# Optimization experiments

Measured on AMD Instinct MI355X. Metric: run time of the kernel, lower is better.

The kernel has to match this reference:

```python
import jax, jax.numpy as jnp
import numpy as np

K_UPPER = 196608  # number of smallest-|grad| positions to mask per sample


def setup_inputs() -> dict:
    key = jax.random.key(0)
    k1, k2 = jax.random.split(key)
    x = jax.random.normal(k1, (64, 3, 512, 512), dtype=jnp.float32)
    grad = jax.random.normal(k2, (64, 3, 512, 512), dtype=jnp.float32)
    return {"x": x, "grad": grad}


def _mask_low_gradient(x, grad):
    # x, grad: [B, C, H, W]
    B, C, H, W = x.shape
    hw = H * W
    flat_g = grad.reshape(B, -1)                                  # [B, C*H*W]
    # _sort: k smallest absolute gradients -> top_k of negated abs (unsorted ok)
    _neg_vals, idx = jax.lax.top_k(-jnp.abs(flat_g), K_UPPER)     # idx: [B, K]
    # channel containing each selected flat index (matches the torch range test)
    ch = idx // hw                                                # [B, K]
    xc = x.reshape(B, C, hw)
    # Faithful to source: torch slice [start:channel_indexes] EXCLUDES the last
    # element of each channel when computing min/max.
    mn = jnp.min(xc[:, :, : hw - 1], axis=-1)                     # [B, C]
    mx = jnp.max(xc[:, :, : hw - 1], axis=-1)                     # [B, C]
    lo = jnp.take_along_axis(mn, ch, axis=1)                      # [B, K]
    hi = jnp.take_along_axis(mx, ch, axis=1)                      # [B, K]
    # uniform fill in [lo, hi) per masked element
    u = jax.random.uniform(jax.random.key(42), idx.shape, dtype=x.dtype)
    fill = lo + u * (hi - lo)                                     # [B, K]
    flat_x = x.reshape(B, -1)
    out = flat_x.at[jnp.arange(B)[:, None], idx].set(fill)
    return out.reshape(x.shape)


def reference(x, grad):
    return _mask_low_gradient(x, grad)
```

## Files before the change

### kernel.cpp

```cpp
#include <hip/hip_runtime.h>
#include <stdint.h>

#define TPB 256
#define TPS 1024

constexpr int BN   = 64;
constexpr int CCH  = 3;
constexpr int HWS  = 262144;
constexpr int LOG_HW = 18;
constexpr int NPS  = 786432;
constexpr int KSEL = 196608;
constexpr int KCAP = 200704;
constexpr int NB_T = 32;
constexpr int CH_T = NPS / NB_T;
constexpr int NB_C = 64;
constexpr int CH_C = NPS / NB_C;
constexpr int NB_S = 8;
constexpr int CH_S = KCAP / NB_S;
constexpr int TILE = 4096;
constexpr int NBINS = 2048;
constexpr int SUB  = 8;

constexpr int WS_MN   = 0;
constexpr int WS_MX   = 192;
constexpr int WS_V1   = 384;
constexpr int WS_B1   = 448;
constexpr int WS_GS   = 512;
constexpr int WS_KP   = 576;
constexpr int WS_CNT  = 640;
constexpr int WS_COFF = WS_CNT + BN * NB_C;
constexpr int WS_MNP  = WS_COFF + BN * NB_C;
constexpr int WS_MXP  = WS_MNP + BN * CCH * SUB;
constexpr int WS_THA  = WS_MXP + BN * CCH * SUB;
constexpr int WS_THB  = WS_THA + BN * NBINS;
constexpr int WS_H0   = WS_THB + BN * NBINS;
constexpr int WS_H1   = WS_H0 + BN * 256 * NB_S;
constexpr int WS_H2   = WS_H1 + BN * 256 * NB_S;
constexpr int WS_H3   = WS_H2 + BN * 256 * NB_S;
constexpr size_t WS_FIX_END = (size_t)WS_H3 + (size_t)BN * 256 * NB_S;
constexpr size_t RECW = (size_t)BN * KCAP * 2;
constexpr size_t WS_NEEDED_BYTES = (WS_FIX_END + 2 * RECW) * 4;

__device__ __forceinline__ unsigned rotl32(unsigned x, int r) { return (x << r) | (x >> (32 - r)); }

__device__ __forceinline__ void tf4(unsigned& x0, unsigned& x1, int a, int b, int c, int d) {
  x0 += x1; x1 = rotl32(x1, a); x1 ^= x0;
  x0 += x1; x1 = rotl32(x1, b); x1 ^= x0;
  x0 += x1; x1 = rotl32(x1, c); x1 ^= x0;
  x0 += x1; x1 = rotl32(x1, d); x1 ^= x0;
}

__device__ __forceinline__ void threefry2x32(unsigned k0, unsigned k1, unsigned c0, unsigned c1,
                                             unsigned& o0, unsigned& o1) {
  const unsigned ks2 = k0 ^ k1 ^ 0x1BD11BDAu;
  unsigned x0 = c0 + k0, x1 = c1 + k1;
  tf4(x0, x1, 13, 15, 26, 6);  x0 += k1;  x1 += ks2 + 1u;
  tf4(x0, x1, 17, 29, 16, 24); x0 += ks2; x1 += k0 + 2u;
  tf4(x0, x1, 13, 15, 26, 6);  x0 += k0;  x1 += k1 + 3u;
  tf4(x0, x1, 17, 29, 16, 24); x0 += k1;  x1 += ks2 + 4u;
  tf4(x0, x1, 13, 15, 26, 6);  x0 += ks2; x1 += k0 + 5u;
  o0 = x0; o1 = x1;
}

__global__ __launch_bounds__(TPB) void k_zero(unsigned* __restrict__ p, int n) {
  int i = blockIdx.x * TPB + threadIdx.x;
  if (i < n) p[i] = 0u;
}

__global__ __launch_bounds__(TPB) void k_mnmx(const float4* __restrict__ x,
                                              unsigned* __restrict__ ws) {
  __shared__ float smn[TPB], smx[TPB];
  const int g = blockIdx.x;
  const int bc = g / SUB, sub = g - bc * SUB;
  const int Q4 = HWS / 4 / SUB;
  const size_t base4 = (size_t)bc * (HWS / 4) + (size_t)sub * Q4;
  const bool last = (sub == SUB - 1);
  const int tid = threadIdx.x;
  float lo = 3.4e38f, hi = -3.4e38f;
  for (int i = tid; i < Q4; i += TPB) {
    float4 v = x[base4 + i];
    if (last && i == Q4 - 1) {
      lo = fminf(lo, fminf(fminf(v.x, v.y), v.z));
      hi = fmaxf(hi, fmaxf(fmaxf(v.x, v.y), v.z));
    } else {
      lo = fminf(lo, fminf(fminf(v.x, v.y), fminf(v.z, v.w)));
      hi = fmaxf(hi, fmaxf(fmaxf(v.x, v.y), fmaxf(v.z, v.w)));
    }
  }
  smn[tid] = lo; smx[tid] = hi; __syncthreads();
  for (int s = TPB / 2; s > 0; s >>= 1) {
    if (tid < s) { smn[tid] = fminf(smn[tid], smn[tid + s]); smx[tid] = fmaxf(smx[tid], smx[tid + s]); }
    __syncthreads();
  }
  if (tid == 0) {
    ((float*)(ws + WS_MNP))[g] = smn[0];
    ((float*)(ws + WS_MXP))[g] = smx[0];
  }
}

__global__ __launch_bounds__(TPB) void k_mnfin(unsigned* __restrict__ ws) {
  const int t = threadIdx.x;
  if (t < BN * CCH) {
    const float* mnp = (const float*)(ws + WS_MNP);
    const float* mxp = (const float*)(ws + WS_MXP);
    float lo = 3.4e38f, hi = -3.4e38f;
    for (int s = 0; s < SUB; ++s) {
      lo = fminf(lo, mnp[t * SUB + s]);
      hi = fmaxf(hi, mxp[t * SUB + s]);
    }
    ((float*)(ws + WS_MN))[t] = lo;
    ((float*)(ws + WS_MX))[t] = hi;
  }
}

__global__ __launch_bounds__(TPB) void k_thrA(const unsigned* __restrict__ gb, unsigned* __restrict__ hist) {
  __shared__ unsigned h[NBINS];
  const int b = blockIdx.y, blk = blockIdx.x, tid = threadIdx.x;
  for (int v = tid; v < NBINS; v += TPB) h[v] = 0u;
  __syncthreads();
  const uint4* g4 = (const uint4*)(gb + (size_t)b * NPS + (size_t)blk * CH_T);
  for (int i = tid; i < CH_T / 4; i += TPB) {
    uint4 v = g4[i];
    atomicAdd(&h[(v.x & 0x7FFFFFFFu) >> 21], 1u);
    atomicAdd(&h[(v.y & 0x7FFFFFFFu) >> 21], 1u);
    atomicAdd(&h[(v.z & 0x7FFFFFFFu) >> 21], 1u);
    atomicAdd(&h[(v.w & 0x7FFFFFFFu) >> 21], 1u);
  }
  __syncthreads();
  unsigned* gh = hist + (size_t)b * NBINS;
  for (int v = tid; v < NBINS; v += TPB) if (h[v]) atomicAdd(&gh[v], h[v]);
}

__global__ __launch_bounds__(TPB) void k_thrB(const unsigned* __restrict__ gb,
                                              unsigned* __restrict__ hist,
                                              const unsigned* __restrict__ ws) {
  __shared__ unsigned h[NBINS];
  const int b = blockIdx.y, blk = blockIdx.x, tid = threadIdx.x;
  for (int v = tid; v < NBINS; v += TPB) h[v] = 0u;
  __syncthreads();
  const unsigned sel = ws[WS_V1 + b];
  const uint4* g4 = (const uint4*)(gb + (size_t)b * NPS + (size_t)blk * CH_T);
  for (int i = tid; i < CH_T / 4; i += TPB) {
    uint4 v = g4[i];
    unsigned a0 = v.x & 0x7FFFFFFFu, a1 = v.y & 0x7FFFFFFFu;
    unsigned a2 = v.z & 0x7FFFFFFFu, a3 = v.w & 0x7FFFFFFFu;
    if ((a0 >> 21) == sel) atomicAdd(&h[(a0 >> 10) & 2047u], 1u);
    if ((a1 >> 21) == sel) atomicAdd(&h[(a1 >> 10) & 2047u], 1u);
    if ((a2 >> 21) == sel) atomicAdd(&h[(a2 >> 10) & 2047u], 1u);
    if ((a3 >> 21) == sel) atomicAdd(&h[(a3 >> 10) & 2047u], 1u);
  }
  __syncthreads();
  unsigned* gh = hist + (size_t)b * NBINS;
  for (int v = tid; v < NBINS; v += TPB) if (h[v]) atomicAdd(&gh[v], h[v]);
}

__global__ __launch_bounds__(TPB) void k_find(const unsigned* __restrict__ hist,
                                              unsigned* __restrict__ ws, int mode) {
  __shared__ unsigned part[TPB];
  const int b = blockIdx.x, tid = threadIdx.x;
  const unsigned* h = hist + (size_t)b * NBINS;
  const int per = NBINS / TPB;
  const unsigned Kt = (mode == 0) ? (unsigned)KSEL : (unsigned)KSEL - ws[WS_B1 + b];
  unsigned vals[8];
  unsigned s = 0;
  for (int j = 0; j < per; ++j) { vals[j] = h[tid * per + j]; s += vals[j]; }
  part[tid] = s; __syncthreads();
  for (int off = 1; off < TPB; off <<= 1) {
    unsigned t = (tid >= off) ? part[tid - off] : 0u;
    __syncthreads(); part[tid] += t; __syncthreads();
  }
  unsigned run = part[tid] - s;
  for (int j = 0; j < per; ++j) {
    const unsigned lo = run, c = vals[j];
    run += c;
    if (lo < Kt && Kt <= run) {
      const unsigned v = (unsigned)(tid * per + j);
      if (mode == 0) {
        ws[WS_V1 + b] = v; ws[WS_B1 + b] = lo;
      } else {
        const unsigned T22 = (ws[WS_V1 + b] << 11) | v;
        ws[WS_GS + b] = (T22 << 10) | 1023u;
        unsigned kp = ws[WS_B1 + b] + lo + c;
        if (kp > (unsigned)KCAP) kp = (unsigned)KCAP;
        ws[WS_KP + b] = kp;
      }
    }
  }
}

__global__ __launch_bounds__(TPB) void k_ccount(const unsigned* __restrict__ gb, unsigned* __restrict__ ws) {
  __shared__ unsigned r[TPB];
  const int b = blockIdx.y, blk = blockIdx.x, tid = threadIdx.x;
  const unsigned G = ws[WS_GS + b];
  const uint4* g4 = (const uint4*)(gb + (size_t)b * NPS + (size_t)blk * CH_C);
  unsigned c = 0;
  for (int i = tid; i < CH_C / 4; i += TPB) {
    uint4 v = g4[i];
    c += (unsigned)((v.x & 0x7FFFFFFFu) <= G) + (unsigned)((v.y & 0x7FFFFFFFu) <= G)
       + (unsigned)((v.z & 0x7FFFFFFFu) <= G) + (unsigned)((v.w & 0x7FFFFFFFu) <= G);
  }
  r[tid] = c; __syncthreads();
  for (int s = TPB / 2; s > 0; s >>= 1) { if (tid < s) r[tid] += r[tid + s]; __syncthreads(); }
  if (tid == 0) ws[WS_CNT + b * NB_C + blk] = r[0];
}

__global__ void k_cscan(unsigned* __restrict__ ws) {
  const int b = blockIdx.x;
  if (threadIdx.x == 0) {
    unsigned run = 0;
    for (int j = 0; j < NB_C; ++j) {
      unsigned t = ws[WS_CNT + b * NB_C + j];
      ws[WS_COFF + b * NB_C + j] = run;
      run += t;
    }
  }
}

__global__ __launch_bounds__(TPB) void k_cscatter(const unsigned* __restrict__ gb,
                                                  const unsigned* __restrict__ ws,
                                                  unsigned* __restrict__ keyArr,
                                                  unsigned* __restrict__ H0) {
  __shared__ unsigned h2[256 * NB_S];
  __shared__ unsigned waveTot[4];
  __shared__ unsigned runBase;
  const int b = blockIdx.y, blk = blockIdx.x, tid = threadIdx.x;
  const int lane = tid & 63, wv = tid >> 6;
  const unsigned G = ws[WS_GS + b];
  for (int e = tid; e < 256 * NB_S; e += TPB) h2[e] = 0u;
  if (tid == 0) runBase = ws[WS_COFF + b * NB_C + blk];
  __syncthreads();
  const uint4* g4 = (const uint4*)(gb + (size_t)b * NPS + (size_t)blk * CH_C);
  unsigned* ka = keyArr + (size_t)b * KCAP;
  for (int t = 0; t < CH_C / 1024; ++t) {
    const uint4 v = g4[t * 256 + tid];
    unsigned k[4] = { v.x & 0x7FFFFFFFu, v.y & 0x7FFFFFFFu, v.z & 0x7FFFFFFFu, v.w & 0x7FFFFFFFu };
    bool s[4];
    unsigned cnt = 0;
#pragma unroll
    for (int c = 0; c < 4; ++c) { s[c] = (k[c] <= G); cnt += (unsigned)s[c]; }
    unsigned incl = cnt;
    for (int off = 1; off < 64; off <<= 1) {
      unsigned u = __shfl_up(incl, off, 64);
      if (lane >= off) incl += u;
    }
    if (lane == 63) waveTot[wv] = incl;
    __syncthreads();
    const unsigned wt0 = waveTot[0], wt1 = waveTot[1], wt2 = waveTot[2], wt3 = waveTot[3];
    unsigned wpre = 0;
    if (wv > 0) wpre += wt0;
    if (wv > 1) wpre += wt1;
    if (wv > 2) wpre += wt2;
    unsigned pos = runBase + wpre + (incl - cnt);
#pragma unroll
    for (int c = 0; c < 4; ++c) {
      if (s[c]) {
        if (pos < (unsigned)KCAP) {
          ka[pos] = k[c];
          atomicAdd(&h2[(k[c] & 255u) * NB_S + pos / (unsigned)CH_S], 1u);
        }
        ++pos;
      }
    }
    __syncthreads();
    if (tid == 0) runBase += wt0 + wt1 + wt2 + wt3;
  }
  __syncthreads();
  unsigned* Hb = H0 + (size_t)b * 256 * NB_S;
  for (int e = tid; e < 256 * NB_S; e += TPB) {
    unsigned c = h2[e];
    if (c) atomicAdd(&Hb[e], c);
  }
}

__global__ __launch_bounds__(TPB) void k_hscan(unsigned* __restrict__ H) {
  __shared__ unsigned wsum[4];
  const int b = blockIdx.x, tid = threadIdx.x;
  const int lane = tid & 63, wv = tid >> 6;
  unsigned* Hb = H + (size_t)b * 256 * NB_S;
  unsigned row[NB_S];
  unsigned run = 0;
#pragma unroll
  for (int k = 0; k < NB_S; ++k) {
    unsigned t = Hb[tid * NB_S + k];
    row[k] = run; run += t;
  }
  unsigned incl = run;
  for (int off = 1; off < 64; off <<= 1) {
    unsigned t = __shfl_up(incl, off, 64);
    if (lane >= off) incl += t;
  }
  if (lane == 63) wsum[wv] = incl;
  __syncthreads();
  unsigned wpre = 0;
  for (int w = 0; w < wv; ++w) wpre += wsum[w];
  const unsigned excl = incl - run + wpre;
#pragma unroll
  for (int k = 0; k < NB_S; ++k) Hb[tid * NB_S + k] = row[k] + excl;
}

template<int MODE>
__global__ __launch_bounds__(TPS) void k_sort8(const unsigned* __restrict__ keyIn,
                                               const uint2* __restrict__ inR,
                                               uint2* __restrict__ outR,
                                               unsigned* __restrict__ fillmap,
                                               const unsigned* __restrict__ Hcur,
                                               unsigned* __restrict__ Hnext,
                                               const unsigned* __restrict__ ws,
                                               int shift) {
  __shared__ unsigned wh[16][256];
  __shared__ unsigned gout[256];
  __shared__ unsigned gbase[256];
  __shared__ unsigned wsum[4];
  __shared__ uint2    stg[(MODE == 2) ? 1 : TILE];
  __shared__ unsigned h2[(MODE == 2) ? 1 : 256 * NB_S];
  const int b = blockIdx.y, blk = blockIdx.x, tid = threadIdx.x;
  const int lane = tid & 63, wv = tid >> 6;
  const unsigned long long ltm = (1ull << lane) - 1ull;
  const unsigned kp = min(ws[WS_KP + b], (unsigned)KCAP);
  const unsigned s0 = (unsigned)blk * CH_S;
  const unsigned s1 = min(s0 + (unsigned)CH_S, kp);
  const unsigned* ki = keyIn + (size_t)b * KCAP;
  const uint2* in = inR + (size_t)b * KCAP;
  uint2* out = outR + (size_t)b * KCAP;
  unsigned* fm = fillmap + (size_t)b * KCAP;

  for (int d = tid; d < 256; d += TPS) gbase[d] = Hcur[((size_t)b * 256 + d) * NB_S + blk];
  if (MODE != 2) for (int e = tid; e < 256 * NB_S; e += TPS) h2[e] = 0u;
  __syncthreads();

  for (unsigned t0 = s0; t0 < s1; t0 += (unsigned)TILE) {
    { uint4* w4 = (uint4*)&wh[0][0];
      w4[tid] = make_uint4(0u, 0u, 0u, 0u); }
    __syncthreads();

    unsigned key[4], cpp[4], wloc[4], dig[4];
    bool val[4];
    const unsigned wbase = t0 + (unsigned)wv * 256u;
#pragma unroll
    for (int c = 0; c < 4; ++c) {
      const unsigned i = wbase + (unsigned)c * 64u + (unsigned)lane;
      val[c] = (i < s1);
      if (MODE == 0) { cpp[c] = i; key[c] = val[c] ? ki[i] : 0u; }
      else { uint2 r = val[c] ? in[i] : make_uint2(0u, 0u); cpp[c] = r.x; key[c] = r.y; }
      dig[c] = (key[c] >> shift) & 255u;
      unsigned long long peers = __ballot(val[c]);
#pragma unroll
      for (int bit = 0; bit < 8; ++bit) {
        unsigned long long bb = __ballot(val[c] && ((dig[c] >> bit) & 1u));
        peers &= ((dig[c] >> bit) & 1u) ? bb : ~bb;
      }
      const unsigned before = (unsigned)__popcll(peers & ltm);
      int ldr = __ffsll((unsigned long long)peers) - 1;
      if (ldr < 0) ldr = 0;
      unsigned old = 0;
      if (val[c] && lane == ldr) old = atomicAdd(&wh[wv][dig[c]], (unsigned)__popcll(peers));
      old = __shfl(old, ldr, 64);
      wloc[c] = old + before;
    }
    __syncthreads();

    unsigned incl = 0, tot = 0;
    if (tid < 256) {
      const unsigned d = (unsigned)tid;
#pragma unroll
      for (int w = 0; w < 16; ++w) tot += wh[w][d];
      incl = tot;
      for (int off = 1; off < 64; off <<= 1) {
        unsigned t = __shfl_up(incl, off, 64);
        if (lane >= off) incl += t;
      }
      if (lane == 63) wsum[wv] = incl;
    }
    __syncthreads();
    if (tid < 256) {
      const unsigned d = (unsigned)tid;
      unsigned wpre = 0;
      for (int w = 0; w < wv; ++w) wpre += wsum[w];
      const unsigned tstart = incl - tot + wpre;
      const unsigned g = gbase[d];
      gout[d] = g - tstart;
      gbase[d] = g + tot;
      unsigned run = tstart;
#pragma unroll
      for (int w = 0; w < 16; ++w) { const unsigned t = wh[w][d]; wh[w][d] = run; run += t; }
    }
    __syncthreads();

    if (MODE != 2) {
#pragma unroll
      for (int c = 0; c < 4; ++c) {
        if (val[c]) {
          uint2 r; r.x = cpp[c]; r.y = key[c];
          stg[wh[wv][dig[c]] + wloc[c]] = r;
        }
      }
      __syncthreads();
      const unsigned nt = min((unsigned)TILE, s1 - t0);
      for (unsigned j = tid; j < nt; j += TPS) {
        const uint2 r = stg[j];
        const unsigned d = (r.y >> shift) & 255u;
        const unsigned pos = gout[d] + j;
        out[pos] = r;
        const unsigned nd = (r.y >> (shift + 8)) & 255u;
        atomicAdd(&h2[nd * NB_S + pos / (unsigned)CH_S], 1u);
      }
    } else {
#pragma unroll
      for (int c = 0; c < 4; ++c) {
        if (val[c]) {
          const unsigned rank = gout[dig[c]] + wh[wv][dig[c]] + wloc[c];
          fm[cpp[c]] = (rank < (unsigned)KSEL) ? rank : 0xFFFFFFFFu;
        }
      }
    }
    __syncthreads();
  }

  if (MODE != 2) {
    unsigned* Hb = Hnext + (size_t)b * 256 * NB_S;
    for (int e = tid; e < 256 * NB_S; e += TPS) {
      unsigned c = h2[e];
      if (c) atomicAdd(&Hb[e], c);
    }
  }
}

__global__ __launch_bounds__(TPB) void k_fill(const uint4* __restrict__ x4,
                                              const unsigned* __restrict__ gb,
                                              const unsigned* __restrict__ fillmap,
                                              const unsigned* __restrict__ ws,
                                              float4* __restrict__ out4) {
  __shared__ unsigned waveTot[4];
  __shared__ unsigned runBase;
  const int b = blockIdx.y, blk = blockIdx.x, tid = threadIdx.x;
  const int lane = tid & 63, wv = tid >> 6;
  const unsigned G = ws[WS_GS + b];
  const unsigned kp = min(ws[WS_KP + b], (unsigned)KCAP);
  if (tid == 0) runBase = ws[WS_COFF + b * NB_C + blk];
  __syncthreads();
  const size_t base4 = ((size_t)b * NPS + (size_t)blk * CH_C) / 4;
  const uint4* g4 = (const uint4*)(gb + (size_t)b * NPS + (size_t)blk * CH_C);
  const unsigned* fm = fillmap + (size_t)b * KCAP;
  const float* mnf = (const float*)(ws + WS_MN);
  const float* mxf = (const float*)(ws + WS_MX);
  const unsigned ebase = (unsigned)blk * (unsigned)CH_C;

  for (int t = 0; t < CH_C / 1024; ++t) {
    const uint4 gv = g4[t * 256 + tid];
    uint4 xv = ((const uint4*)x4)[base4 + t * 256 + tid];
    unsigned k[4] = { gv.x & 0x7FFFFFFFu, gv.y & 0x7FFFFFFFu, gv.z & 0x7FFFFFFFu, gv.w & 0x7FFFFFFFu };
    bool s[4];
    unsigned cnt = 0;
#pragma unroll
    for (int c = 0; c < 4; ++c) { s[c] = (k[c] <= G); cnt += (unsigned)s[c]; }
    unsigned incl = cnt;
    for (int off = 1; off < 64; off <<= 1) {
      unsigned u = __shfl_up(incl, off, 64);
      if (lane >= off) incl += u;
    }
    if (lane == 63) waveTot[wv] = incl;
    __syncthreads();
    const unsigned wt0 = waveTot[0], wt1 = waveTot[1], wt2 = waveTot[2], wt3 = waveTot[3];
    unsigned wpre = 0;
    if (wv > 0) wpre += wt0;
    if (wv > 1) wpre += wt1;
    if (wv > 2) wpre += wt2;
    unsigned pos = runBase + wpre + (incl - cnt);
    unsigned* xw = (unsigned*)&xv;
#pragma unroll
    for (int c = 0; c < 4; ++c) {
      if (s[c]) {
        if (pos < kp) {
          const unsigned r = fm[pos];
          if (r != 0xFFFFFFFFu) {
            const unsigned p = (unsigned)b * (unsigned)KSEL + r;
            unsigned o0, o1;
            threefry2x32(0u, 42u, 0u, p, o0, o1);
            const unsigned bits = o0 ^ o1;
            const float u = __uint_as_float((bits >> 9) | 0x3f800000u) - 1.0f;
            const unsigned e = ebase + (unsigned)t * 1024u + (unsigned)tid * 4u + (unsigned)c;
            const unsigned ch = e >> LOG_HW;
            const float lo = mnf[b * CCH + ch];
            const float hi = mxf[b * CCH + ch];
            xw[c] = __float_as_uint(lo + u * (hi - lo));
          }
        }
        ++pos;
      }
    }
    ((uint4*)out4)[base4 + t * 256 + tid] = xv;
    __syncthreads();
    if (tid == 0) runBase += wt0 + wt1 + wt2 + wt3;
  }
}

extern "C" void kernel_launch(void* const* d_in, const int* in_sizes, int n_in,
                              void* d_out, int out_size, void* d_ws, size_t ws_size,
                              hipStream_t stream) {
  const float* x = (const float*)d_in[0];
  const unsigned* gb = (const unsigned*)d_in[1];
  float* out = (float*)d_out;
  unsigned* ws = (unsigned*)d_ws;
  if (ws_size < WS_NEEDED_BYTES) return;

  unsigned* R1 = ws + WS_FIX_END;
  unsigned* R2 = ws + WS_FIX_END + RECW;
  unsigned* H0 = ws + WS_H0;
  unsigned* H1 = ws + WS_H1;
  unsigned* H2 = ws + WS_H2;
  unsigned* H3 = ws + WS_H3;

  dim3 blk(TPB);
  dim3 sblk(TPS);

  k_mnmx<<<dim3(BN * CCH * SUB), blk, 0, stream>>>((const float4*)x, ws);
  k_mnfin<<<dim3(1), blk, 0, stream>>>(ws);
  {
    const int nz = (int)(WS_FIX_END - WS_THA);
    k_zero<<<dim3((nz + TPB - 1) / TPB), blk, 0, stream>>>(ws + WS_THA, nz);
  }

  k_thrA<<<dim3(NB_T, BN), blk, 0, stream>>>(gb, ws + WS_THA);
  k_find<<<dim3(BN), blk, 0, stream>>>(ws + WS_THA, ws, 0);
  k_thrB<<<dim3(NB_T, BN), blk, 0, stream>>>(gb, ws + WS_THB, ws);
  k_find<<<dim3(BN), blk, 0, stream>>>(ws + WS_THB, ws, 1);

  k_ccount<<<dim3(NB_C, BN), blk, 0, stream>>>(gb, ws);
  k_cscan<<<dim3(BN), dim3(64), 0, stream>>>(ws);
  k_cscatter<<<dim3(NB_C, BN), blk, 0, stream>>>(gb, ws, R1, H0);

  k_hscan<<<dim3(BN), blk, 0, stream>>>(H0);
  k_sort8<0><<<dim3(NB_S, BN), sblk, 0, stream>>>(R1, (const uint2*)nullptr, (uint2*)R2, nullptr, H0, H1, ws, 0);
  k_hscan<<<dim3(BN), blk, 0, stream>>>(H1);
  k_sort8<1><<<dim3(NB_S, BN), sblk, 0, stream>>>(nullptr, (const uint2*)R2, (uint2*)R1, nullptr, H1, H2, ws, 8);
  k_hscan<<<dim3(BN), blk, 0, stream>>>(H2);
  k_sort8<1><<<dim3(NB_S, BN), sblk, 0, stream>>>(nullptr, (const uint2*)R1, (uint2*)R2, nullptr, H2, H3, ws, 16);
  k_hscan<<<dim3(BN), blk, 0, stream>>>(H3);
  k_sort8<2><<<dim3(NB_S, BN), sblk, 0, stream>>>(nullptr, (const uint2*)R2, (uint2*)nullptr, R1, H3, nullptr, ws, 24);

  k_fill<<<dim3(NB_C, BN), blk, 0, stream>>>((const uint4*)x, gb, R1, ws, (float4*)out);
}
```

Before: 798.2 us.

## Use per-wave compaction offsets and compute fill values in final sort pass

Compaction now gives each wave its own contiguous sub-chunk with a precomputed offset. This removes the two block-wide barriers per iteration in the scatter and fill kernels, and the single-thread scan becomes a parallel 256-entry scan. The threefry RNG and lo/hi fill computation move from k_fill into the last sort pass (MODE 2), which writes the final float value into the fillmap. Per-channel selected counts are accumulated so the sort pass can find each element's channel from its compacted position. This adds atomics in k_ccount and more arithmetic in the sort kernel, but k_fill becomes a plain memory-bound merge.

Result: faster. 779.5 us (-2.3%).

```diff
diff --git a/kernel.cpp b/kernel.cpp
--- a/kernel.cpp
+++ b/kernel.cpp
@@ -15,6 +15,7 @@
 constexpr int CH_T = NPS / NB_T;
 constexpr int NB_C = 64;
 constexpr int CH_C = NPS / NB_C;
+constexpr int WCH  = CH_C / 4;
 constexpr int NB_S = 8;
 constexpr int CH_S = KCAP / NB_S;
 constexpr int TILE = 4096;
@@ -27,11 +28,14 @@
 constexpr int WS_B1   = 448;
 constexpr int WS_GS   = 512;
 constexpr int WS_KP   = 576;
-constexpr int WS_CNT  = 640;
-constexpr int WS_COFF = WS_CNT + BN * NB_C;
-constexpr int WS_MNP  = WS_COFF + BN * NB_C;
+constexpr int WS_S0   = 640;
+constexpr int WS_S01  = 704;
+constexpr int WS_CNT  = 768;
+constexpr int WS_COFF = WS_CNT + BN * 256;
+constexpr int WS_MNP  = WS_COFF + BN * 256;
 constexpr int WS_MXP  = WS_MNP + BN * CCH * SUB;
-constexpr int WS_THA  = WS_MXP + BN * CCH * SUB;
+constexpr int WS_CHC  = WS_MXP + BN * CCH * SUB;
+constexpr int WS_THA  = WS_CHC + BN * 4;
 constexpr int WS_THB  = WS_THA + BN * NBINS;
 constexpr int WS_H0   = WS_THB + BN * NBINS;
 constexpr int WS_H1   = WS_H0 + BN * 256 * NB_S;
@@ -189,30 +193,56 @@
 }
 
 __global__ __launch_bounds__(TPB) void k_ccount(const unsigned* __restrict__ gb, unsigned* __restrict__ ws) {
-  __shared__ unsigned r[TPB];
+  __shared__ unsigned chs[3];
   const int b = blockIdx.y, blk = blockIdx.x, tid = threadIdx.x;
+  const int lane = tid & 63, wv = tid >> 6;
+  if (tid < 3) chs[tid] = 0u;
+  __syncthreads();
   const unsigned G = ws[WS_GS + b];
-  const uint4* g4 = (const uint4*)(gb + (size_t)b * NPS + (size_t)blk * CH_C);
-  unsigned c = 0;
-  for (int i = tid; i < CH_C / 4; i += TPB) {
-    uint4 v = g4[i];
-    c += (unsigned)((v.x & 0x7FFFFFFFu) <= G) + (unsigned)((v.y & 0x7FFFFFFFu) <= G)
-       + (unsigned)((v.z & 0x7FFFFFFFu) <= G) + (unsigned)((v.w & 0x7FFFFFFFu) <= G);
-  }
-  r[tid] = c; __syncthreads();
-  for (int s = TPB / 2; s > 0; s >>= 1) { if (tid < s) r[tid] += r[tid + s]; __syncthreads(); }
-  if (tid == 0) ws[WS_CNT + b * NB_C + blk] = r[0];
-}
-
-__global__ void k_cscan(unsigned* __restrict__ ws) {
-  const int b = blockIdx.x;
-  if (threadIdx.x == 0) {
-    unsigned run = 0;
-    for (int j = 0; j < NB_C; ++j) {
-      unsigned t = ws[WS_CNT + b * NB_C + j];
-      ws[WS_COFF + b * NB_C + j] = run;
-      run += t;
-    }
+  const uint4* g4 = (const uint4*)(gb + (size_t)b * NPS + (size_t)blk * CH_C) + wv * (WCH / 4);
+  const unsigned e0 = (unsigned)blk * CH_C + (unsigned)wv * WCH;
+  unsigned cnt = 0, cc0 = 0, cc1 = 0, cc2 = 0;
+  for (int it = 0; it < WCH / 256; ++it) {
+    const uint4 v = g4[it * 64 + lane];
+    const unsigned e = e0 + (unsigned)it * 256u + (unsigned)lane * 4u;
+    const unsigned k[4] = { v.x & 0x7FFFFFFFu, v.y & 0x7FFFFFFFu, v.z & 0x7FFFFFFFu, v.w & 0x7FFFFFFFu };
+#pragma unroll
+    for (int c = 0; c < 4; ++c) {
+      if (k[c] <= G) {
+        ++cnt;
+        const unsigned ch = (e + (unsigned)c) >> LOG_HW;
+        if (ch == 0) ++cc0; else if (ch == 1) ++cc1; else ++cc2;
+      }
+    }
+  }
+  for (int off = 32; off >= 1; off >>= 1) cnt += __shfl_down(cnt, off, 64);
+  if (lane == 0) ws[WS_CNT + b * 256 + blk * 4 + wv] = cnt;
+  if (cc0) atomicAdd(&chs[0], cc0);
+  if (cc1) atomicAdd(&chs[1], cc1);
+  if (cc2) atomicAdd(&chs[2], cc2);
+  __syncthreads();
+  if (tid < 3 && chs[tid]) atomicAdd(&ws[WS_CHC + b * 4 + tid], chs[tid]);
+}
+
+__global__ __launch_bounds__(TPB) void k_cscan(unsigned* __restrict__ ws) {
+  __shared__ unsigned wsum[4];
+  const int b = blockIdx.x, tid = threadIdx.x;
+  const int lane = tid & 63, wv = tid >> 6;
+  const unsigned cnt = ws[WS_CNT + b * 256 + tid];
+  unsigned incl = cnt;
+  for (int off = 1; off < 64; off <<= 1) {
+    unsigned t = __shfl_up(incl, off, 64);
+    if (lane >= off) incl += t;
+  }
+  if (lane == 63) wsum[wv] = incl;
+  __syncthreads();
+  unsigned wpre = 0;
+  for (int w = 0; w < wv; ++w) wpre += wsum[w];
+  ws[WS_COFF + b * 256 + tid] = incl - cnt + wpre;
+  if (tid == 0) {
+    const unsigned s0 = ws[WS_CHC + b * 4 + 0];
+    ws[WS_S0 + b] = s0;
+    ws[WS_S01 + b] = s0 + ws[WS_CHC + b * 4 + 1];
   }
 }
 
@@ -221,18 +251,16 @@
                                                   unsigned* __restrict__ keyArr,
                                                   unsigned* __restrict__ H0) {
   __shared__ unsigned h2[256 * NB_S];
-  __shared__ unsigned waveTot[4];
-  __shared__ unsigned runBase;
   const int b = blockIdx.y, blk = blockIdx.x, tid = threadIdx.x;
   const int lane = tid & 63, wv = tid >> 6;
+  for (int e = tid; e < 256 * NB_S; e += TPB) h2[e] = 0u;
+  __syncthreads();
   const unsigned G = ws[WS_GS + b];
-  for (int e = tid; e < 256 * NB_S; e += TPB) h2[e] = 0u;
-  if (tid == 0) runBase = ws[WS_COFF + b * NB_C + blk];
-  __syncthreads();
-  const uint4* g4 = (const uint4*)(gb + (size_t)b * NPS + (size_t)blk * CH_C);
+  unsigned base = ws[WS_COFF + b * 256 + blk * 4 + wv];
+  const uint4* g4 = (const uint4*)(gb + (size_t)b * NPS + (size_t)blk * CH_C) + wv * (WCH / 4);
   unsigned* ka = keyArr + (size_t)b * KCAP;
-  for (int t = 0; t < CH_C / 1024; ++t) {
-    const uint4 v = g4[t * 256 + tid];
+  for (int it = 0; it < WCH / 256; ++it) {
+    const uint4 v = g4[it * 64 + lane];
     unsigned k[4] = { v.x & 0x7FFFFFFFu, v.y & 0x7FFFFFFFu, v.z & 0x7FFFFFFFu, v.w & 0x7FFFFFFFu };
     bool s[4];
     unsigned cnt = 0;
@@ -243,14 +271,8 @@
       unsigned u = __shfl_up(incl, off, 64);
       if (lane >= off) incl += u;
     }
-    if (lane == 63) waveTot[wv] = incl;
-    __syncthreads();
-    const unsigned wt0 = waveTot[0], wt1 = waveTot[1], wt2 = waveTot[2], wt3 = waveTot[3];
-    unsigned wpre = 0;
-    if (wv > 0) wpre += wt0;
-    if (wv > 1) wpre += wt1;
-    if (wv > 2) wpre += wt2;
-    unsigned pos = runBase + wpre + (incl - cnt);
+    const unsigned wtot = __shfl(incl, 63, 64);
+    unsigned pos = base + incl - cnt;
 #pragma unroll
     for (int c = 0; c < 4; ++c) {
       if (s[c]) {
@@ -261,8 +283,7 @@
         ++pos;
       }
     }
-    __syncthreads();
-    if (tid == 0) runBase += wt0 + wt1 + wt2 + wt3;
+    base += wtot;
   }
   __syncthreads();
   unsigned* Hb = H0 + (size_t)b * 256 * NB_S;
@@ -324,6 +345,16 @@
   uint2* out = outR + (size_t)b * KCAP;
   unsigned* fm = fillmap + (size_t)b * KCAP;
 
+  unsigned S0 = 0, S01 = 0;
+  float l0 = 0, l1 = 0, l2 = 0, h0 = 0, h1 = 0, h2v = 0;
+  if (MODE == 2) {
+    S0 = ws[WS_S0 + b]; S01 = ws[WS_S01 + b];
+    const float* mnf = (const float*)(ws + WS_MN);
+    const float* mxf = (const float*)(ws + WS_MX);
+    l0 = mnf[b * CCH]; l1 = mnf[b * CCH + 1]; l2 = mnf[b * CCH + 2];
+    h0 = mxf[b * CCH]; h1 = mxf[b * CCH + 1]; h2v = mxf[b * CCH + 2];
+  }
+
   for (int d = tid; d < 256; d += TPS) gbase[d] = Hcur[((size_t)b * 256 + d) * NB_S + blk];
   if (MODE != 2) for (int e = tid; e < 256 * NB_S; e += TPS) h2[e] = 0u;
   __syncthreads();
@@ -409,7 +440,19 @@
       for (int c = 0; c < 4; ++c) {
         if (val[c]) {
           const unsigned rank = gout[dig[c]] + wh[wv][dig[c]] + wloc[c];
-          fm[cpp[c]] = (rank < (unsigned)KSEL) ? rank : 0xFFFFFFFFu;
+          unsigned res = 0xFFFFFFFFu;
+          if (rank < (unsigned)KSEL) {
+            const unsigned p = (unsigned)b * (unsigned)KSEL + rank;
+            unsigned o0, o1;
+            threefry2x32(0u, 42u, 0u, p, o0, o1);
+            const unsigned bits = o0 ^ o1;
+            const float u = __uint_as_float((bits >> 9) | 0x3f800000u) - 1.0f;
+            const unsigned ch = (unsigned)(cpp[c] >= S0) + (unsigned)(cpp[c] >= S01);
+            const float lo = (ch == 0) ? l0 : ((ch == 1) ? l1 : l2);
+            const float hi = (ch == 0) ? h0 : ((ch == 1) ? h1 : h2v);
+            res = __float_as_uint(lo + u * (hi - lo));
+          }
+          fm[cpp[c]] = res;
         }
       }
     }
@@ -429,25 +472,18 @@
                                               const unsigned* __restrict__ gb,
                                               const unsigned* __restrict__ fillmap,
                                               const unsigned* __restrict__ ws,
-                                              float4* __restrict__ out4) {
-  __shared__ unsigned waveTot[4];
-  __shared__ unsigned runBase;
+                                              uint4* __restrict__ out4) {
   const int b = blockIdx.y, blk = blockIdx.x, tid = threadIdx.x;
   const int lane = tid & 63, wv = tid >> 6;
   const unsigned G = ws[WS_GS + b];
   const unsigned kp = min(ws[WS_KP + b], (unsigned)KCAP);
-  if (tid == 0) runBase = ws[WS_COFF + b * NB_C + blk];
-  __syncthreads();
-  const size_t base4 = ((size_t)b * NPS + (size_t)blk * CH_C) / 4;
-  const uint4* g4 = (const uint4*)(gb + (size_t)b * NPS + (size_t)blk * CH_C);
+  unsigned base = ws[WS_COFF + b * 256 + blk * 4 + wv];
+  const size_t t4 = (size_t)b * (NPS / 4) + (size_t)blk * (CH_C / 4) + (size_t)wv * (WCH / 4);
   const unsigned* fm = fillmap + (size_t)b * KCAP;
-  const float* mnf = (const float*)(ws + WS_MN);
-  const float* mxf = (const float*)(ws + WS_MX);
-  const unsigned ebase = (unsigned)blk * (unsigned)CH_C;
-
-  for (int t = 0; t < CH_C / 1024; ++t) {
-    const uint4 gv = g4[t * 256 + tid];
-    uint4 xv = ((const uint4*)x4)[base4 + t * 256 + tid];
+  for (int it = 0; it < WCH / 256; ++it) {
+    const size_t a = t4 + it * 64 + lane;
+    const uint4 gv = ((const uint4*)gb)[a];
+    uint4 xv = x4[a];
     unsigned k[4] = { gv.x & 0x7FFFFFFFu, gv.y & 0x7FFFFFFFu, gv.z & 0x7FFFFFFFu, gv.w & 0x7FFFFFFFu };
     bool s[4];
     unsigned cnt = 0;
@@ -458,39 +494,21 @@
       unsigned u = __shfl_up(incl, off, 64);
       if (lane >= off) incl += u;
     }
-    if (lane == 63) waveTot[wv] = incl;
-    __syncthreads();
-    const unsigned wt0 = waveTot[0], wt1 = waveTot[1], wt2 = waveTot[2], wt3 = waveTot[3];
-    unsigned wpre = 0;
-    if (wv > 0) wpre += wt0;
-    if (wv > 1) wpre += wt1;
-    if (wv > 2) wpre += wt2;
-    unsigned pos = runBase + wpre + (incl - cnt);
+    const unsigned wtot = __shfl(incl, 63, 64);
+    unsigned pos = base + incl - cnt;
     unsigned* xw = (unsigned*)&xv;
 #pragma unroll
     for (int c = 0; c < 4; ++c) {
       if (s[c]) {
         if (pos < kp) {
           const unsigned r = fm[pos];
-          if (r != 0xFFFFFFFFu) {
-            const unsigned p = (unsigned)b * (unsigned)KSEL + r;
-            unsigned o0, o1;
-            threefry2x32(0u, 42u, 0u, p, o0, o1);
-            const unsigned bits = o0 ^ o1;
-            const float u = __uint_as_float((bits >> 9) | 0x3f800000u) - 1.0f;
-            const unsigned e = ebase + (unsigned)t * 1024u + (unsigned)tid * 4u + (unsigned)c;
-            const unsigned ch = e >> LOG_HW;
-            const float lo = mnf[b * CCH + ch];
-            const float hi = mxf[b * CCH + ch];
-            xw[c] = __float_as_uint(lo + u * (hi - lo));
-          }
+          if (r != 0xFFFFFFFFu) xw[c] = r;
         }
         ++pos;
       }
     }
-    ((uint4*)out4)[base4 + t * 256 + tid] = xv;
-    __syncthreads();
-    if (tid == 0) runBase += wt0 + wt1 + wt2 + wt3;
+    out4[a] = xv;
+    base += wtot;
   }
 }
 
@@ -516,8 +534,8 @@
   k_mnmx<<<dim3(BN * CCH * SUB), blk, 0, stream>>>((const float4*)x, ws);
   k_mnfin<<<dim3(1), blk, 0, stream>>>(ws);
   {
-    const int nz = (int)(WS_FIX_END - WS_THA);
-    k_zero<<<dim3((nz + TPB - 1) / TPB), blk, 0, stream>>>(ws + WS_THA, nz);
+    const int nz = (int)(WS_FIX_END - WS_CHC);
+    k_zero<<<dim3((nz + TPB - 1) / TPB), blk, 0, stream>>>(ws + WS_CHC, nz);
   }
 
   k_thrA<<<dim3(NB_T, BN), blk, 0, stream>>>(gb, ws + WS_THA);
@@ -526,7 +544,7 @@
   k_find<<<dim3(BN), blk, 0, stream>>>(ws + WS_THB, ws, 1);
 
   k_ccount<<<dim3(NB_C, BN), blk, 0, stream>>>(gb, ws);
-  k_cscan<<<dim3(BN), dim3(64), 0, stream>>>(ws);
+  k_cscan<<<dim3(BN), blk, 0, stream>>>(ws);
   k_cscatter<<<dim3(NB_C, BN), blk, 0, stream>>>(gb, ws, R1, H0);
 
   k_hscan<<<dim3(BN), blk, 0, stream>>>(H0);
@@ -538,5 +556,5 @@
   k_hscan<<<dim3(BN), blk, 0, stream>>>(H3);
   k_sort8<2><<<dim3(NB_S, BN), sblk, 0, stream>>>(nullptr, (const uint2*)R2, (uint2*)nullptr, R1, H3, nullptr, ws, 24);
 
-  k_fill<<<dim3(NB_C, BN), blk, 0, stream>>>((const uint4*)x, gb, R1, ws, (float4*)out);
-}
+  k_fill<<<dim3(NB_C, BN), blk, 0, stream>>>((const uint4*)x, gb, R1, ws, (uint4*)out);
+}
```
